# Performance work log

Measured on AMD Instinct MI355X. Metric: run time of the kernel, lower is better.

The kernel has to match this reference:

```python
import jax, jax.numpy as jnp
import numpy as np

N_NODES = 25000
N_EDGES = 400000
H = 128
EPS = 1e-8


def _mlp(x, W1, b1, W2, b2):
    # Linear -> silu -> Linear (PaiNN context network, blocks=2)
    return jax.nn.silu(x @ W1 + b1) @ W2 + b2


def setup_inputs() -> dict:
    key = jax.random.key(0)
    ks = jax.random.split(key, 16)
    d = {}
    d["s"] = jax.random.normal(ks[0], (N_NODES, 1, H), dtype=jnp.float32)
    d["v"] = jax.random.normal(ks[1], (N_NODES, 3, H), dtype=jnp.float32)
    d["dir_ij"] = jax.random.normal(ks[2], (N_EDGES, 3), dtype=jnp.float32)
    d["Wij"] = jax.random.normal(ks[3], (N_EDGES, 1, 3 * H), dtype=jnp.float32) * 0.1
    # interaction block params: Linear(H) -> silu -> Linear(3H)
    d["Wi1"] = jax.random.normal(ks[4], (H, H), dtype=jnp.float32) / np.sqrt(H)
    d["bi1"] = jnp.zeros((H,), dtype=jnp.float32)
    d["Wi2"] = jax.random.normal(ks[5], (H, 3 * H), dtype=jnp.float32) / np.sqrt(H)
    d["bi2"] = jnp.zeros((3 * H,), dtype=jnp.float32)
    # mixing block params: input is concat(s, v_norm) -> 2H features
    d["Wm1"] = jax.random.normal(ks[6], (2 * H, H), dtype=jnp.float32) / np.sqrt(2 * H)
    d["bm1"] = jnp.zeros((H,), dtype=jnp.float32)
    d["Wm2"] = jax.random.normal(ks[7], (H, 3 * H), dtype=jnp.float32) / np.sqrt(H)
    d["bm2"] = jnp.zeros((3 * H,), dtype=jnp.float32)
    # vector mixing block: Linear(2H), no bias
    d["Wv"] = jax.random.normal(ks[8], (H, 2 * H), dtype=jnp.float32) / np.sqrt(H)
    d["senders"] = jax.random.randint(ks[9], (N_EDGES,), 0, N_NODES, dtype=jnp.int32)
    d["receivers"] = jax.random.randint(ks[10], (N_EDGES,), 0, N_NODES, dtype=jnp.int32)
    return d


def reference(s, v, dir_ij, Wij, Wi1, bi1, Wi2, bi2, Wm1, bm1, Wm2, bm2, Wv,
              senders, receivers):
    n_nodes = s.shape[0]
    # ---- message (inter-particle) ----
    x = _mlp(s, Wi1, bi1, Wi2, bi2)              # (n, 1, 3H)
    xj = x[receivers]                            # (e, 1, 3H)
    vj = v[receivers]                            # (e, 3, H)
    ds_e, dv1, dv2 = jnp.split(Wij * xj, 3, axis=-1)   # each (e, 1, H)
    dv_e = dv1 * dir_ij[..., jnp.newaxis] + dv2 * vj   # (e, 3, H)
    ds = jax.ops.segment_sum(ds_e, senders, num_segments=n_nodes)
    dv = jax.ops.segment_sum(dv_e, senders, num_segments=n_nodes)
    s = s + jnp.clip(ds, -100.0, 100.0)
    v = v + jnp.clip(dv, -100.0, 100.0)
    # ---- update (intra-particle) ----
    v_l, v_r = jnp.split(v @ Wv, 2, axis=-1)     # each (n, 3, H)
    v_norm = jnp.sqrt(jnp.sum(v_r ** 2, axis=-2, keepdims=True) + EPS)  # (n, 1, H)
    ts = jnp.concatenate([s, v_norm], axis=-1)   # (n, 1, 2H)
    ds_u, dv_u, dsv = jnp.split(_mlp(ts, Wm1, bm1, Wm2, bm2), 3, axis=-1)
    dv_u = v_l * dv_u                            # (n, 3, H)
    dsv = dsv * jnp.sum(v_r * v_l, axis=1, keepdims=True)  # (n, 1, H)
    s = s + jnp.clip(ds_u + dsv, -100.0, 100.0)
    v = v + jnp.clip(dv_u, -100.0, 100.0)
    return (s, v)
```

## Files before the change

### kernel.cpp

```cpp
#include <hip/hip_runtime.h>
#include <cstddef>

#define NNODES 25000
#define NEDGES 400000

__device__ __forceinline__ float clip100(float x) {
    return fminf(fmaxf(x, -100.0f), 100.0f);
}
__device__ __forceinline__ float silu_f(float x) {
    return x / (1.0f + __expf(-x));
}

__global__ __launch_bounds__(256, 4) void k_node_mlp(
    const float* __restrict__ s,
    const float* __restrict__ Wi1, const float* __restrict__ bi1,
    const float* __restrict__ Wi2, const float* __restrict__ bi2,
    float* __restrict__ x)
{
    __shared__ __align__(16) float s_lds[8][128];
    __shared__ __align__(16) float h_lds[8][128];
    const int tid = threadIdx.x;
    const int g = tid >> 6;
    const int l = tid & 63;
    const int n0 = 2 * g, n1 = n0 + 1;
    const long gn0 = (long)blockIdx.x * 8 + n0;
    const long gn1 = gn0 + 1;

    #pragma unroll
    for (int i = 0; i < 2; ++i) {
        int h = l + 64 * i;
        s_lds[n0][h] = s[gn0 * 128 + h];
        s_lds[n1][h] = s[gn1 * 128 + h];
    }

    float accA[2][2];
    accA[0][0] = accA[1][0] = bi1[l];
    accA[0][1] = accA[1][1] = bi1[l + 64];
    #pragma unroll 4
    for (int k = 0; k < 128; ++k) {
        float w0 = Wi1[k * 128 + l];
        float w1 = Wi1[k * 128 + l + 64];
        float i0 = s_lds[n0][k];
        float i1 = s_lds[n1][k];
        accA[0][0] = fmaf(i0, w0, accA[0][0]);
        accA[0][1] = fmaf(i0, w1, accA[0][1]);
        accA[1][0] = fmaf(i1, w0, accA[1][0]);
        accA[1][1] = fmaf(i1, w1, accA[1][1]);
    }
    h_lds[n0][l]      = silu_f(accA[0][0]);
    h_lds[n0][l + 64] = silu_f(accA[0][1]);
    h_lds[n1][l]      = silu_f(accA[1][0]);
    h_lds[n1][l + 64] = silu_f(accA[1][1]);

    float accB[2][6];
    #pragma unroll
    for (int i = 0; i < 6; ++i) {
        float b = bi2[l + 64 * i];
        accB[0][i] = b; accB[1][i] = b;
    }
    #pragma unroll 4
    for (int k = 0; k < 128; ++k) {
        float i0 = h_lds[n0][k];
        float i1 = h_lds[n1][k];
        #pragma unroll
        for (int i = 0; i < 6; ++i) {
            float w = Wi2[k * 384 + l + 64 * i];
            accB[0][i] = fmaf(i0, w, accB[0][i]);
            accB[1][i] = fmaf(i1, w, accB[1][i]);
        }
    }
    #pragma unroll
    for (int i = 0; i < 6; ++i) {
        x[gn0 * 384 + l + 64 * i] = accB[0][i];
        x[gn1 * 384 + l + 64 * i] = accB[1][i];
    }
}

__global__ __launch_bounds__(256, 4) void k_edge(
    const float* __restrict__ x, const float* __restrict__ v,
    const float* __restrict__ dir_ij, const float* __restrict__ Wij,
    const int* __restrict__ senders, const int* __restrict__ receivers,
    float* __restrict__ acc)
{
    const long e = (long)blockIdx.x * 2 + (threadIdx.x >> 7);
    const int h = threadIdx.x & 127;
    const int se = senders[e];
    const int re = receivers[e];
    const float d0 = dir_ij[e * 3 + 0];
    const float d1 = dir_ij[e * 3 + 1];
    const float d2 = dir_ij[e * 3 + 2];
    const float* __restrict__ wrow = Wij + e * 384;
    const float* __restrict__ xrow = x + (long)re * 384;
    const float* __restrict__ vrow = v + (long)re * 384;

    float ds = wrow[h]       * xrow[h];
    float a  = wrow[128 + h] * xrow[128 + h];
    float b  = wrow[256 + h] * xrow[256 + h];
    float dv0 = fmaf(a, d0, b * vrow[h]);
    float dv1 = fmaf(a, d1, b * vrow[128 + h]);
    float dv2 = fmaf(a, d2, b * vrow[256 + h]);

    float* arow = acc + (long)se * 512;
    unsafeAtomicAdd(arow + h,       ds);
    unsafeAtomicAdd(arow + 128 + h, dv0);
    unsafeAtomicAdd(arow + 256 + h, dv1);
    unsafeAtomicAdd(arow + 384 + h, dv2);
}

__global__ __launch_bounds__(256, 4) void k_update(
    const float* __restrict__ s_in, const float* __restrict__ v_in,
    const float* __restrict__ acc,
    const float* __restrict__ Wm1, const float* __restrict__ bm1,
    const float* __restrict__ Wm2, const float* __restrict__ bm2,
    const float* __restrict__ Wv,
    float* __restrict__ s_out, float* __restrict__ v_out)
{
    __shared__ __align__(16) float ts[8][256];
    __shared__ __align__(16) float v_cur[8][384];
    __shared__ __align__(16) float hid[8][128];
    const int tid = threadIdx.x;
    const int g = tid >> 6;
    const int l = tid & 63;
    const int n0 = 2 * g, n1 = n0 + 1;
    const long gn0 = (long)blockIdx.x * 8 + n0;
    const long gn1 = gn0 + 1;

    #pragma unroll
    for (int i = 0; i < 2; ++i) {
        int h = l + 64 * i;
        ts[n0][h] = s_in[gn0 * 128 + h] + clip100(acc[gn0 * 512 + h]);
        ts[n1][h] = s_in[gn1 * 128 + h] + clip100(acc[gn1 * 512 + h]);
    }
    float vreg[2][6];
    #pragma unroll
    for (int i = 0; i < 6; ++i) {
        int r = l + 64 * i;
        vreg[0][i] = v_in[gn0 * 384 + r] + clip100(acc[gn0 * 512 + 128 + r]);
        vreg[1][i] = v_in[gn1 * 384 + r] + clip100(acc[gn1 * 512 + 128 + r]);
        v_cur[n0][r] = vreg[0][i];
        v_cur[n1][r] = vreg[1][i];
    }

    float aV[2][3][4];
    #pragma unroll
    for (int j = 0; j < 2; ++j)
        #pragma unroll
        for (int d = 0; d < 3; ++d)
            #pragma unroll
            for (int i = 0; i < 4; ++i) aV[j][d][i] = 0.0f;
    #pragma unroll 4
    for (int k = 0; k < 128; ++k) {
        float w[4];
        #pragma unroll
        for (int i = 0; i < 4; ++i) w[i] = Wv[k * 256 + l + 64 * i];
        #pragma unroll
        for (int d = 0; d < 3; ++d) {
            float i0 = v_cur[n0][d * 128 + k];
            float i1 = v_cur[n1][d * 128 + k];
            #pragma unroll
            for (int i = 0; i < 4; ++i) {
                aV[0][d][i] = fmaf(i0, w[i], aV[0][d][i]);
                aV[1][d][i] = fmaf(i1, w[i], aV[1][d][i]);
            }
        }
    }

    float vv[2][2];
    #pragma unroll
    for (int j = 0; j < 2; ++j) {
        int nn = (j == 0) ? n0 : n1;
        #pragma unroll
        for (int i = 0; i < 2; ++i) {
            int h = l + 64 * i;
            float l0 = aV[j][0][i],     l1 = aV[j][1][i],     l2 = aV[j][2][i];
            float r0 = aV[j][0][i + 2], r1 = aV[j][1][i + 2], r2 = aV[j][2][i + 2];
            ts[nn][128 + h] = sqrtf(fmaf(r0, r0, fmaf(r1, r1, r2 * r2)) + 1e-8f);
            vv[j][i] = fmaf(r0, l0, fmaf(r1, l1, r2 * l2));
        }
    }

    float aM[2][2];
    aM[0][0] = aM[1][0] = bm1[l];
    aM[0][1] = aM[1][1] = bm1[l + 64];
    #pragma unroll 4
    for (int k = 0; k < 256; ++k) {
        float w0 = Wm1[k * 128 + l];
        float w1 = Wm1[k * 128 + l + 64];
        float i0 = ts[n0][k];
        float i1 = ts[n1][k];
        aM[0][0] = fmaf(i0, w0, aM[0][0]);
        aM[0][1] = fmaf(i0, w1, aM[0][1]);
        aM[1][0] = fmaf(i1, w0, aM[1][0]);
        aM[1][1] = fmaf(i1, w1, aM[1][1]);
    }
    hid[n0][l]      = silu_f(aM[0][0]);
    hid[n0][l + 64] = silu_f(aM[0][1]);
    hid[n1][l]      = silu_f(aM[1][0]);
    hid[n1][l + 64] = silu_f(aM[1][1]);

    float aB[2][6];
    #pragma unroll
    for (int i = 0; i < 6; ++i) {
        float b = bm2[l + 64 * i];
        aB[0][i] = b; aB[1][i] = b;
    }
    #pragma unroll 4
    for (int k = 0; k < 128; ++k) {
        float i0 = hid[n0][k];
        float i1 = hid[n1][k];
        #pragma unroll
        for (int i = 0; i < 6; ++i) {
            float w = Wm2[k * 384 + l + 64 * i];
            aB[0][i] = fmaf(i0, w, aB[0][i]);
            aB[1][i] = fmaf(i1, w, aB[1][i]);
        }
    }

    #pragma unroll
    for (int j = 0; j < 2; ++j) {
        int nn = (j == 0) ? n0 : n1;
        long gn = (j == 0) ? gn0 : gn1;
        #pragma unroll
        for (int i = 0; i < 2; ++i) {
            int h = l + 64 * i;
            s_out[gn * 128 + h] = ts[nn][h] + clip100(aB[j][i] + aB[j][4 + i] * vv[j][i]);
        }
        #pragma unroll
        for (int i = 0; i < 6; ++i) {
            int r = l + 64 * i;
            int d = i >> 1;
            int b = i & 1;
            float vl = aV[j][d][b];
            float dvu = aB[j][2 + b];
            v_out[gn * 384 + r] = vreg[j][i] + clip100(vl * dvu);
        }
    }
}

extern "C" void kernel_launch(void* const* d_in, const int* in_sizes, int n_in,
                              void* d_out, int out_size, void* d_ws, size_t ws_size,
                              hipStream_t stream) {
    const float* s   = (const float*)d_in[0];
    const float* v   = (const float*)d_in[1];
    const float* dir = (const float*)d_in[2];
    const float* Wij = (const float*)d_in[3];
    const float* Wi1 = (const float*)d_in[4];
    const float* bi1 = (const float*)d_in[5];
    const float* Wi2 = (const float*)d_in[6];
    const float* bi2 = (const float*)d_in[7];
    const float* Wm1 = (const float*)d_in[8];
    const float* bm1 = (const float*)d_in[9];
    const float* Wm2 = (const float*)d_in[10];
    const float* bm2 = (const float*)d_in[11];
    const float* Wv  = (const float*)d_in[12];
    const int* senders   = (const int*)d_in[13];
    const int* receivers = (const int*)d_in[14];

    float* xbuf = (float*)d_ws;
    float* accb = xbuf + (size_t)NNODES * 384;
    float* s_out = (float*)d_out;
    float* v_out = s_out + (size_t)NNODES * 128;

    hipMemsetAsync(accb, 0, (size_t)NNODES * 512 * sizeof(float), stream);
    k_node_mlp<<<NNODES / 8, 256, 0, stream>>>(s, Wi1, bi1, Wi2, bi2, xbuf);
    k_edge<<<NEDGES / 2, 256, 0, stream>>>(xbuf, v, dir, Wij, senders, receivers, accb);
    k_update<<<NNODES / 8, 256, 0, stream>>>(s, v, accb, Wm1, bm1, Wm2, bm2, Wv,
                                             s_out, v_out);
}
```

Baseline: 1.646 ms.

## Replace atomic edge scatter with CSR-sorted per-node gather accumulation

Builds a CSR index of edges grouped by sender using histogram, scan and scatter kernels, then processes each node with one wavefront that sums its incoming edge contributions in registers and writes once. This removes the 1.6M-element float atomic traffic and the accumulator memset. In exchange it adds three preprocessing launches, including a single-block serial scan, and edge reads become indirect through eids, which can hurt coalescing of the Wij rows.

```diff
diff --git a/kernel.cpp b/kernel.cpp
--- a/kernel.cpp
+++ b/kernel.cpp
@@ -9,6 +9,54 @@
 }
 __device__ __forceinline__ float silu_f(float x) {
     return x / (1.0f + __expf(-x));
+}
+
+__global__ void k_hist(const int* __restrict__ senders, int* __restrict__ counts)
+{
+    int e = blockIdx.x * 256 + threadIdx.x;
+    if (e < NEDGES) atomicAdd(&counts[senders[e]], 1);
+}
+
+__global__ void k_scan(const int* __restrict__ counts,
+                       int* __restrict__ rowstart, int* __restrict__ cursor)
+{
+    __shared__ int buf[1024];
+    __shared__ int carry_s;
+    const int tid = threadIdx.x;
+    if (tid == 0) carry_s = 0;
+    __syncthreads();
+    const int nchunks = (NNODES + 1023) / 1024;
+    for (int c = 0; c < nchunks; ++c) {
+        int i = c * 1024 + tid;
+        int val = (i < NNODES) ? counts[i] : 0;
+        buf[tid] = val;
+        __syncthreads();
+        #pragma unroll
+        for (int off = 1; off < 1024; off <<= 1) {
+            int t = (tid >= off) ? buf[tid - off] : 0;
+            __syncthreads();
+            buf[tid] += t;
+            __syncthreads();
+        }
+        int incl = buf[tid];
+        int excl = incl - val + carry_s;
+        if (i < NNODES) { rowstart[i] = excl; cursor[i] = excl; }
+        int chunk_total = buf[1023];
+        __syncthreads();
+        if (tid == 0) carry_s += chunk_total;
+        __syncthreads();
+    }
+    if (tid == 0) rowstart[NNODES] = carry_s;
+}
+
+__global__ void k_scatter(const int* __restrict__ senders,
+                          int* __restrict__ cursor, int* __restrict__ eids)
+{
+    int e = blockIdx.x * 256 + threadIdx.x;
+    if (e < NEDGES) {
+        int pos = atomicAdd(&cursor[senders[e]], 1);
+        eids[pos] = e;
+    }
 }
 
 __global__ __launch_bounds__(256, 4) void k_node_mlp(
@@ -76,35 +124,58 @@
     }
 }
 
-__global__ __launch_bounds__(256, 4) void k_edge(
+__global__ __launch_bounds__(256, 8) void k_edge_sorted(
     const float* __restrict__ x, const float* __restrict__ v,
     const float* __restrict__ dir_ij, const float* __restrict__ Wij,
-    const int* __restrict__ senders, const int* __restrict__ receivers,
+    const int* __restrict__ receivers,
+    const int* __restrict__ rowstart, const int* __restrict__ eids,
     float* __restrict__ acc)
 {
-    const long e = (long)blockIdx.x * 2 + (threadIdx.x >> 7);
-    const int h = threadIdx.x & 127;
-    const int se = senders[e];
-    const int re = receivers[e];
-    const float d0 = dir_ij[e * 3 + 0];
-    const float d1 = dir_ij[e * 3 + 1];
-    const float d2 = dir_ij[e * 3 + 2];
-    const float* __restrict__ wrow = Wij + e * 384;
-    const float* __restrict__ xrow = x + (long)re * 384;
-    const float* __restrict__ vrow = v + (long)re * 384;
-
-    float ds = wrow[h]       * xrow[h];
-    float a  = wrow[128 + h] * xrow[128 + h];
-    float b  = wrow[256 + h] * xrow[256 + h];
-    float dv0 = fmaf(a, d0, b * vrow[h]);
-    float dv1 = fmaf(a, d1, b * vrow[128 + h]);
-    float dv2 = fmaf(a, d2, b * vrow[256 + h]);
-
-    float* arow = acc + (long)se * 512;
-    unsafeAtomicAdd(arow + h,       ds);
-    unsafeAtomicAdd(arow + 128 + h, dv0);
-    unsafeAtomicAdd(arow + 256 + h, dv1);
-    unsafeAtomicAdd(arow + 384 + h, dv2);
+    const int wave = threadIdx.x >> 6;
+    const int l = threadIdx.x & 63;
+    const int n = blockIdx.x * 4 + wave;
+    if (n >= NNODES) return;
+
+    float ds0 = 0.0f, ds1 = 0.0f;
+    float dva0 = 0.0f, dva1 = 0.0f, dva2 = 0.0f;
+    float dvb0 = 0.0f, dvb1 = 0.0f, dvb2 = 0.0f;
+
+    const int jb = rowstart[n];
+    const int je = rowstart[n + 1];
+    for (int j = jb; j < je; ++j) {
+        const int e  = eids[j];
+        const int re = receivers[e];
+        const float* __restrict__ wr = Wij + (long)e * 384;
+        const float* __restrict__ xr = x + (long)re * 384;
+        const float* __restrict__ vr = v + (long)re * 384;
+        const float d0 = dir_ij[e * 3 + 0];
+        const float d1 = dir_ij[e * 3 + 1];
+        const float d2 = dir_ij[e * 3 + 2];
+
+        float w0a = wr[l],       w1a = wr[128 + l], w2a = wr[256 + l];
+        float w0b = wr[64 + l],  w1b = wr[192 + l], w2b = wr[320 + l];
+        float x0a = xr[l],       x1a = xr[128 + l], x2a = xr[256 + l];
+        float x0b = xr[64 + l],  x1b = xr[192 + l], x2b = xr[320 + l];
+        float va0 = vr[l],       va1 = vr[128 + l], va2 = vr[256 + l];
+        float vb0 = vr[64 + l],  vb1 = vr[192 + l], vb2 = vr[320 + l];
+
+        ds0 = fmaf(w0a, x0a, ds0);
+        ds1 = fmaf(w0b, x0b, ds1);
+        float aa = w1a * x1a, ba = w2a * x2a;
+        float ab = w1b * x1b, bb = w2b * x2b;
+        dva0 = fmaf(aa, d0, fmaf(ba, va0, dva0));
+        dva1 = fmaf(aa, d1, fmaf(ba, va1, dva1));
+        dva2 = fmaf(aa, d2, fmaf(ba, va2, dva2));
+        dvb0 = fmaf(ab, d0, fmaf(bb, vb0, dvb0));
+        dvb1 = fmaf(ab, d1, fmaf(bb, vb1, dvb1));
+        dvb2 = fmaf(ab, d2, fmaf(bb, vb2, dvb2));
+    }
+
+    float* __restrict__ arow = acc + (long)n * 512;
+    arow[l]        = ds0;   arow[64 + l]  = ds1;
+    arow[128 + l]  = dva0;  arow[192 + l] = dvb0;
+    arow[256 + l]  = dva1;  arow[320 + l] = dvb1;
+    arow[384 + l]  = dva2;  arow[448 + l] = dvb2;
 }
 
 __global__ __launch_bounds__(256, 4) void k_update(
@@ -258,12 +329,20 @@
 
     float* xbuf = (float*)d_ws;
     float* accb = xbuf + (size_t)NNODES * 384;
+    int* counts   = (int*)(accb + (size_t)NNODES * 512);
+    int* rowstart = counts + NNODES;
+    int* cursor   = rowstart + NNODES + 8;
+    int* eids     = cursor + NNODES;
     float* s_out = (float*)d_out;
     float* v_out = s_out + (size_t)NNODES * 128;
 
-    hipMemsetAsync(accb, 0, (size_t)NNODES * 512 * sizeof(float), stream);
+    hipMemsetAsync(counts, 0, (size_t)NNODES * sizeof(int), stream);
+    k_hist<<<(NEDGES + 255) / 256, 256, 0, stream>>>(senders, counts);
+    k_scan<<<1, 1024, 0, stream>>>(counts, rowstart, cursor);
+    k_scatter<<<(NEDGES + 255) / 256, 256, 0, stream>>>(senders, cursor, eids);
     k_node_mlp<<<NNODES / 8, 256, 0, stream>>>(s, Wi1, bi1, Wi2, bi2, xbuf);
-    k_edge<<<NEDGES / 2, 256, 0, stream>>>(xbuf, v, dir, Wij, senders, receivers, accb);
+    k_edge_sorted<<<(NNODES + 3) / 4, 256, 0, stream>>>(
+        xbuf, v, dir, Wij, receivers, rowstart, eids, accb);
     k_update<<<NNODES / 8, 256, 0, stream>>>(s, v, accb, Wm1, bm1, Wm2, bm2, Wv,
                                              s_out, v_out);
 }
```

Result: faster. 1.377 ms (-16.3%).
